# Performance work log

Measured on AMD Instinct MI355X. Metric: run time of the kernel, lower is better.

Reference implementation:

```python
import jax, jax.numpy as jnp
import numpy as np

B_, L_, DM = 2, 2048, 1024
DS, DC, EXP, HD = 128, 4, 2, 64
DI = EXP * DM              # 2048
NH = DI // HD              # 32 heads
CONV_DIM = DI + 2 * DS     # 2304
DIN = 2 * DI + 2 * DS + NH # 4384 (z, xBC, dt)
CS = 256                   # SSD chunk size
EPS = 1e-5


def setup_inputs() -> dict:
    key = jax.random.key(0)
    ks = jax.random.split(key, 8)
    s = 0.02
    x = jax.random.normal(ks[0], (B_, L_, DM), jnp.float32)
    norm_w = jnp.ones((DM,), jnp.float32)
    in_proj_w = jax.random.normal(ks[1], (DIN, DM), jnp.float32) * s
    conv_w = jax.random.normal(ks[2], (CONV_DIM, DC), jnp.float32) * 0.2
    conv_b = jnp.zeros((CONV_DIM,), jnp.float32)
    # inverse-softplus of dt ~ U(0.001, 0.1)
    dt_bias = jnp.log(jnp.expm1(jax.random.uniform(ks[3], (NH,), minval=0.001, maxval=0.1)))
    A_log = jnp.log(jax.random.uniform(ks[4], (NH,), minval=1.0, maxval=16.0))
    D = jnp.ones((NH,), jnp.float32)
    gnorm_w = jnp.ones((DI,), jnp.float32)
    out_proj_w = jax.random.normal(ks[5], (DM, DI), jnp.float32) * s
    return dict(x=x, norm_w=norm_w, in_proj_w=in_proj_w, conv_w=conv_w, conv_b=conv_b,
                dt_bias=dt_bias, A_log=A_log, D=D, gnorm_w=gnorm_w, out_proj_w=out_proj_w)


def _segsum(a):
    # a: [..., T] -> [..., T, T]; (i,j) = sum_{j<k<=i} a_k, -inf above diagonal
    T = a.shape[-1]
    cs = jnp.cumsum(a, -1)
    seg = cs[..., :, None] - cs[..., None, :]
    mask = jnp.tril(jnp.ones((T, T), bool))
    return jnp.where(mask, seg, -jnp.inf)


def _ssd(X, A, Bm, Cm):
    # X: [b,l,h,p] (= x*dt), A: [b,l,h] (= dt*a), Bm,Cm: [b,l,n] (ngroups=1)
    b, l, h, p = X.shape
    n, nc = Bm.shape[-1], l // CS
    X = X.reshape(b, nc, CS, h, p)
    A = A.reshape(b, nc, CS, h).transpose(0, 3, 1, 2)  # [b,h,c,s]
    Bm = Bm.reshape(b, nc, CS, n)
    Cm = Cm.reshape(b, nc, CS, n)
    Acs = jnp.cumsum(A, -1)                            # [b,h,c,s]
    Lmat = jnp.exp(_segsum(A))                         # [b,h,c,s,s]
    Y_diag = jnp.einsum('bcln,bcsn,bhcls,bcshp->bclhp', Cm, Bm, Lmat, X)
    decay_states = jnp.exp(Acs[..., -1:] - Acs)        # [b,h,c,s]
    states = jnp.einsum('bcln,bhcl,bclhp->bchpn', Bm, decay_states, X)
    states = jnp.concatenate([jnp.zeros_like(states[:, :1]), states], axis=1)  # [b,c+1,h,p,n]
    decay_chunk = jnp.exp(_segsum(jnp.pad(Acs[..., -1], ((0, 0), (0, 0), (1, 0)))))  # [b,h,c+1,c+1]
    states = jnp.einsum('bhzc,bchpn->bzhpn', decay_chunk, states)[:, :-1]
    Y_off = jnp.einsum('bcln,bchpn,bhcl->bclhp', Cm, states, jnp.exp(Acs))
    return (Y_diag + Y_off).reshape(b, l, h, p)


def _forward(x, norm_w, in_proj_w, conv_w, conv_b, dt_bias, A_log, D, gnorm_w, out_proj_w):
    b, l, _ = x.shape
    # outer RMSNorm
    xn = x * jax.lax.rsqrt(jnp.mean(x * x, -1, keepdims=True) + EPS) * norm_w
    zxbcdt = jnp.einsum('bld,ed->ble', xn, in_proj_w)
    z = zxbcdt[..., :DI]
    xBC = zxbcdt[..., DI:DI + CONV_DIM]
    dt = zxbcdt[..., -NH:]
    # causal depthwise conv1d + bias + silu
    pad = jnp.pad(xBC, ((0, 0), (DC - 1, 0), (0, 0)))
    conv = sum(pad[:, k:k + l, :] * conv_w[:, k] for k in range(DC)) + conv_b
    xBC = conv * jax.nn.sigmoid(conv)
    xs = xBC[..., :DI]
    Bm = xBC[..., DI:DI + DS]
    Cm = xBC[..., DI + DS:]
    dt = jax.nn.softplus(dt + dt_bias)                 # [b,l,h]
    A = -jnp.exp(A_log)                                # [h]
    xh = xs.reshape(b, l, NH, HD)
    y = _ssd(xh * dt[..., None], dt * A, Bm, Cm)
    y = y + D[None, None, :, None] * xh
    y = y.reshape(b, l, DI)
    # gated RMSNorm (norm_before_gate=False): rmsnorm(y * silu(z)) * w
    y = y * (z * jax.nn.sigmoid(z))
    y = y * jax.lax.rsqrt(jnp.mean(y * y, -1, keepdims=True) + EPS) * gnorm_w
    return x + jnp.einsum('bld,ed->ble', y, out_proj_w)


def reference(x, norm_w, in_proj_w, conv_w, conv_b, dt_bias, A_log, D, gnorm_w, out_proj_w):
    return _forward(x, norm_w, in_proj_w, conv_w, conv_b, dt_bias, A_log, D, gnorm_w, out_proj_w)
```

## Files before the change

### kernel.cpp

```cpp
#include <hip/hip_runtime.h>
#include <hip/hip_bf16.h>

#define BB      2
#define LSEQ    2048
#define DMODEL  1024
#define DSTATE  128
#define DCONV   4
#define HEADDIM 64
#define DINNER  2048
#define NHEADS  32
#define CONVD   2304
#define DINP    4384
#define CHUNK   256
#define NCH     8
#define NROWS   4096
#define EPSF    1e-5f
#define TPAD    264
#define WIPAD   4480

typedef __attribute__((ext_vector_type(8))) short bf16x8;
typedef __attribute__((ext_vector_type(4))) float f32x4;

#define ASYNC_COPY16(gptr, lptr) \
    __builtin_amdgcn_global_load_lds((const __attribute__((address_space(1))) void*)(gptr), \
                                     (__attribute__((address_space(3))) void*)(lptr), 16, 0, 0)

__device__ __forceinline__ ushort f2bf(float f) {
    __hip_bfloat16 h = __float2bfloat16(f);
    return *(ushort*)&h;
}
__device__ __forceinline__ float bf2f(ushort u) {
    return __uint_as_float(((unsigned)u) << 16);
}
__device__ __forceinline__ short fb(float f) { return (short)f2bf(f); }
__device__ __forceinline__ short tb(float f) { return (short)(__float_as_uint(f) >> 16); }

__global__ __launch_bounds__(256) void prologue_kernel(
    const float* __restrict__ x, const float* __restrict__ norm_w,
    const float* __restrict__ in_proj_w, const float* __restrict__ out_proj_w,
    const float* __restrict__ gnorm_w,
    ushort* __restrict__ xn_bf, ushort* __restrict__ wi_bf,
    ushort* __restrict__ wo_bf, float* __restrict__ ssq)
{
    int bid = blockIdx.x;
    if (bid < 4480) {
        long i4 = ((long)bid * 256 + threadIdx.x) * 4;
        int n = (int)(i4 >> 10);
        long k = i4 & 1023;
        ushort4 o;
        if (n < DINP) {
            float4 v = *(const float4*)(in_proj_w + ((long)n << 10) + k);
            o.x = f2bf(v.x); o.y = f2bf(v.y); o.z = f2bf(v.z); o.w = f2bf(v.w);
        } else { o.x = o.y = o.z = o.w = 0; }
        *(ushort4*)(wi_bf + i4) = o;
    } else if (bid < 6528) {
        long i4 = ((long)(bid - 4480) * 256 + threadIdx.x) * 4;
        int k = (int)(i4 & 2047);
        float4 v = *(const float4*)(out_proj_w + i4);
        float4 g = *(const float4*)(gnorm_w + k);
        ushort4 o;
        o.x = f2bf(v.x * g.x); o.y = f2bf(v.y * g.y);
        o.z = f2bf(v.z * g.z); o.w = f2bf(v.w * g.w);
        *(ushort4*)(wo_bf + i4) = o;
    } else if (bid < 10624) {
        int row = bid - 6528;
        const float* xr = x + (long)row * DMODEL;
        float4 v = *(const float4*)(xr + threadIdx.x * 4);
        float ss = v.x*v.x + v.y*v.y + v.z*v.z + v.w*v.w;
        for (int off = 32; off; off >>= 1) ss += __shfl_down(ss, off, 64);
        __shared__ float red[4];
        if ((threadIdx.x & 63) == 0) red[threadIdx.x >> 6] = ss;
        __syncthreads();
        float tot = red[0] + red[1] + red[2] + red[3];
        float scale = rsqrtf(tot / (float)DMODEL + EPSF);
        float4 wv = *(const float4*)(norm_w + threadIdx.x * 4);
        ushort4 o;
        o.x = f2bf(v.x * scale * wv.x); o.y = f2bf(v.y * scale * wv.y);
        o.z = f2bf(v.z * scale * wv.z); o.w = f2bf(v.w * scale * wv.w);
        *(ushort4*)(xn_bf + (long)row * DMODEL + threadIdx.x * 4) = o;
    } else {
        ssq[(bid - 10624) * 256 + threadIdx.x] = 0.f;
    }
}

__global__ __launch_bounds__(256, 3) void gemm_bf16_kernel(
    const ushort* __restrict__ A, int lda, long sA,
    const ushort* __restrict__ W, int ldw, long sW,
    void* __restrict__ Cout, int ldc, long sC, int c_bf16,
    const float* __restrict__ resid, const float* __restrict__ rowscale,
    int mtiles, int ntiles, int N, int K)
{
    __shared__ __align__(16) char smem[34816];
    ushort* As = (ushort*)smem;
    ushort* Bs = As + 128 * 64;
    ushort* tu = (ushort*)smem;
    float*  tf = (float*)smem;

    const int t = threadIdx.x;
    const int lane = t & 63;
    const int w = t >> 6;
    const int wm = w & 1, wn = w >> 1;
    const int lm = lane & 15, quad = lane >> 4;

    int pid = blockIdx.x;
    const int GM = 8;
    int width = GM * ntiles;
    int group = pid / width;
    int first_m = group * GM;
    int gsz = mtiles - first_m; if (gsz > GM) gsz = GM;
    int mt = first_m + (pid % width) % gsz;
    int nt = (pid % width) / gsz;
    const int m0 = mt * 128, n0 = nt * 128;

    A += (long)blockIdx.z * sA;
    W += (long)blockIdx.z * sW;

    const ushort* ga[4]; const ushort* gw[4];
#pragma unroll
    for (int i = 0; i < 4; ++i) {
        int s = i * 256 + t;
        int row = s >> 3;
        int kseg = (s & 7) ^ (row & 7);
        ga[i] = A + (long)(m0 + row) * lda + kseg * 8;
        gw[i] = W + (long)(n0 + row) * ldw + kseg * 8;
    }

    f32x4 acc[4][4];
    f32x4 zero4 = {0.f, 0.f, 0.f, 0.f};
#pragma unroll
    for (int i = 0; i < 4; ++i)
#pragma unroll
        for (int j = 0; j < 4; ++j) acc[i][j] = zero4;

    int arow8[4], arow7[4], brow8[4], brow7[4];
#pragma unroll
    for (int i = 0; i < 4; ++i) {
        int ar = wm * 64 + i * 16 + lm;
        arow8[i] = ar * 8; arow7[i] = ar & 7;
        int br = wn * 64 + i * 16 + lm;
        brow8[i] = br * 8; brow7[i] = br & 7;
    }

    for (int k0 = 0; k0 < K; k0 += 64) {
#pragma unroll
        for (int i = 0; i < 4; ++i) {
            ASYNC_COPY16(ga[i], &As[(i * 256 + w * 64) * 8]);
            ga[i] += 64;
        }
#pragma unroll
        for (int i = 0; i < 4; ++i) {
            ASYNC_COPY16(gw[i], &Bs[(i * 256 + w * 64) * 8]);
            gw[i] += 64;
        }
        __syncthreads();
#pragma unroll
        for (int ks = 0; ks < 2; ++ks) {
            bf16x8 af[4], bfr[4];
#pragma unroll
            for (int i = 0; i < 4; ++i)
                af[i]  = *(const bf16x8*)&As[(arow8[i] + ((ks * 4 + quad) ^ arow7[i])) * 8];
#pragma unroll
            for (int i = 0; i < 4; ++i)
                bfr[i] = *(const bf16x8*)&Bs[(brow8[i] + ((ks * 4 + quad) ^ brow7[i])) * 8];
#pragma unroll
            for (int im = 0; im < 4; ++im)
#pragma unroll
                for (int in = 0; in < 4; ++in)
                    acc[im][in] = __builtin_amdgcn_mfma_f32_16x16x32_bf16(
                        af[im], bfr[in], acc[im][in], 0, 0, 0);
        }
        __syncthreads();
    }

    if (c_bf16) {
        ushort* C = (ushort*)Cout + (long)blockIdx.z * sC;
#pragma unroll
        for (int mi = 0; mi < 4; ++mi)
#pragma unroll
            for (int ni = 0; ni < 4; ++ni) {
                int c = wn * 64 + ni * 16 + lm;
#pragma unroll
                for (int i = 0; i < 4; ++i) {
                    int r = wm * 64 + mi * 16 + quad * 4 + i;
                    tu[r * 136 + c] = f2bf(acc[mi][ni][i]);
                }
            }
        __syncthreads();
        int r = t >> 1, cb = (t & 1) * 64;
        long rowbase = (long)(m0 + r) * ldc + n0 + cb;
#pragma unroll
        for (int q = 0; q < 8; ++q) {
            int gcol = n0 + cb + q * 8;
            if (gcol < N)
                *(bf16x8*)(C + rowbase + q * 8) =
                    *(const bf16x8*)&tu[r * 136 + cb + q * 8];
        }
    } else {
        float* C = (float*)Cout + (long)blockIdx.z * sC;
#pragma unroll
        for (int p = 0; p < 2; ++p) {
            if (wm == p) {
#pragma unroll
                for (int mi = 0; mi < 4; ++mi)
#pragma unroll
                    for (int i = 0; i < 4; ++i) {
                        int r = mi * 16 + quad * 4 + i;
                        float s = 1.f;
                        if (rowscale)
                            s = rsqrtf(rowscale[m0 + p * 64 + r] * (1.f / (float)DINNER) + EPSF);
#pragma unroll
                        for (int ni = 0; ni < 4; ++ni) {
                            int c = wn * 64 + ni * 16 + lm;
                            tf[r * 132 + c] = acc[mi][ni][i] * s;
                        }
                    }
            }
            __syncthreads();
            int r2 = t >> 2, cb = (t & 3) * 32;
            long gbase = (long)(m0 + p * 64 + r2) * ldc + n0 + cb;
#pragma unroll
            for (int q = 0; q < 8; ++q) {
                float4 v = *(const float4*)&tf[r2 * 132 + cb + q * 4];
                if (resid) {
                    float4 rv = *(const float4*)(resid + gbase + q * 4);
                    v.x += rv.x; v.y += rv.y; v.z += rv.z; v.w += rv.w;
                }
                *(float4*)(C + gbase + q * 4) = v;
            }
            __syncthreads();
        }
    }
}

__global__ __launch_bounds__(256, 4) void gemm_bf16_s_kernel(
    const ushort* __restrict__ A, int lda, long sA,
    const ushort* __restrict__ W, int ldw, long sW,
    void* __restrict__ Cout, int ldc, long sC, int c_bf16,
    const float* __restrict__ resid, const float* __restrict__ rowscale,
    int mtiles, int ntiles, int N, int K)
{
    __shared__ __align__(16) char smem[24576];
    ushort* As = (ushort*)smem;
    ushort* Bs = As + 128 * 64;
    ushort* tu = (ushort*)smem;
    float*  tf = (float*)smem;

    const int t = threadIdx.x;
    const int lane = t & 63;
    const int w = t >> 6;
    const int wm = w & 1, wn = w >> 1;
    const int lm = lane & 15, quad = lane >> 4;

    int pid = blockIdx.x;
    const int GM = 8;
    int width = GM * ntiles;
    int group = pid / width;
    int first_m = group * GM;
    int gsz = mtiles - first_m; if (gsz > GM) gsz = GM;
    int mt = first_m + (pid % width) % gsz;
    int nt = (pid % width) / gsz;
    const int m0 = mt * 128, n0 = nt * 64;

    A += (long)blockIdx.z * sA;
    W += (long)blockIdx.z * sW;

    const ushort* ga[4]; const ushort* gw[2];
#pragma unroll
    for (int i = 0; i < 4; ++i) {
        int s = i * 256 + t;
        int row = s >> 3;
        int kseg = (s & 7) ^ (row & 7);
        ga[i] = A + (long)(m0 + row) * lda + kseg * 8;
    }
#pragma unroll
    for (int i = 0; i < 2; ++i) {
        int s = i * 256 + t;
        int row = s >> 3;
        int kseg = (s & 7) ^ (row & 7);
        gw[i] = W + (long)(n0 + row) * ldw + kseg * 8;
    }

    f32x4 acc[4][2];
    f32x4 zero4 = {0.f, 0.f, 0.f, 0.f};
#pragma unroll
    for (int i = 0; i < 4; ++i) { acc[i][0] = zero4; acc[i][1] = zero4; }

    int arow8[4], arow7[4], brow8[2], brow7[2];
#pragma unroll
    for (int i = 0; i < 4; ++i) {
        int ar = wm * 64 + i * 16 + lm;
        arow8[i] = ar * 8; arow7[i] = ar & 7;
    }
#pragma unroll
    for (int i = 0; i < 2; ++i) {
        int br = wn * 32 + i * 16 + lm;
        brow8[i] = br * 8; brow7[i] = br & 7;
    }

    for (int k0 = 0; k0 < K; k0 += 64) {
#pragma unroll
        for (int i = 0; i < 4; ++i) {
            ASYNC_COPY16(ga[i], &As[(i * 256 + w * 64) * 8]);
            ga[i] += 64;
        }
#pragma unroll
        for (int i = 0; i < 2; ++i) {
            ASYNC_COPY16(gw[i], &Bs[(i * 256 + w * 64) * 8]);
            gw[i] += 64;
        }
        __syncthreads();
#pragma unroll
        for (int ks = 0; ks < 2; ++ks) {
            bf16x8 af[4], bfr[2];
#pragma unroll
            for (int i = 0; i < 4; ++i)
                af[i]  = *(const bf16x8*)&As[(arow8[i] + ((ks * 4 + quad) ^ arow7[i])) * 8];
#pragma unroll
            for (int i = 0; i < 2; ++i)
                bfr[i] = *(const bf16x8*)&Bs[(brow8[i] + ((ks * 4 + quad) ^ brow7[i])) * 8];
#pragma unroll
            for (int im = 0; im < 4; ++im)
#pragma unroll
                for (int in = 0; in < 2; ++in)
                    acc[im][in] = __builtin_amdgcn_mfma_f32_16x16x32_bf16(
                        af[im], bfr[in], acc[im][in], 0, 0, 0);
        }
        __syncthreads();
    }

    if (c_bf16) {
        ushort* C = (ushort*)Cout + (long)blockIdx.z * sC;
#pragma unroll
        for (int mi = 0; mi < 4; ++mi)
#pragma unroll
            for (int ni = 0; ni < 2; ++ni) {
                int c = wn * 32 + ni * 16 + lm;
#pragma unroll
                for (int i = 0; i < 4; ++i) {
                    int r = wm * 64 + mi * 16 + quad * 4 + i;
                    tu[r * 72 + c] = f2bf(acc[mi][ni][i]);
                }
            }
        __syncthreads();
        int r = t >> 1, cb = (t & 1) * 32;
        long rowbase = (long)(m0 + r) * ldc + n0 + cb;
#pragma unroll
        for (int q = 0; q < 4; ++q) {
            int gcol = n0 + cb + q * 8;
            if (gcol < N)
                *(bf16x8*)(C + rowbase + q * 8) =
                    *(const bf16x8*)&tu[r * 72 + cb + q * 8];
        }
    } else {
        float* C = (float*)Cout + (long)blockIdx.z * sC;
#pragma unroll
        for (int p = 0; p < 2; ++p) {
            if (wm == p) {
#pragma unroll
                for (int mi = 0; mi < 4; ++mi)
#pragma unroll
                    for (int i = 0; i < 4; ++i) {
                        int r = mi * 16 + quad * 4 + i;
                        float s = 1.f;
                        if (rowscale)
                            s = rsqrtf(rowscale[m0 + p * 64 + r] * (1.f / (float)DINNER) + EPSF);
#pragma unroll
                        for (int ni = 0; ni < 2; ++ni) {
                            int c = wn * 32 + ni * 16 + lm;
                            tf[r * 68 + c] = acc[mi][ni][i] * s;
                        }
                    }
            }
            __syncthreads();
            int r2 = t >> 2, cb = (t & 3) * 16;
            long gbase = (long)(m0 + p * 64 + r2) * ldc + n0 + cb;
#pragma unroll
            for (int q = 0; q < 4; ++q) {
                float4 v = *(const float4*)&tf[r2 * 68 + cb + q * 4];
                if (resid) {
                    float4 rv = *(const float4*)(resid + gbase + q * 4);
                    v.x += rv.x; v.y += rv.y; v.z += rv.z; v.w += rv.w;
                }
                *(float4*)(C + gbase + q * 4) = v;
            }
            __syncthreads();
        }
    }
}

__device__ __forceinline__ void conv8_row(
    const ushort* __restrict__ zx, const float* __restrict__ cw,
    const float* __restrict__ cb, ushort* __restrict__ xBC_bf,
    int row, int l, int c)
{
    float4 cwv[8];
#pragma unroll
    for (int j = 0; j < 8; ++j) cwv[j] = *(const float4*)(cw + (c + j) * 4);
    float acc[8];
    {
        float4 b0 = *(const float4*)(cb + c);
        float4 b1 = *(const float4*)(cb + c + 4);
        acc[0] = b0.x; acc[1] = b0.y; acc[2] = b0.z; acc[3] = b0.w;
        acc[4] = b1.x; acc[5] = b1.y; acc[6] = b1.z; acc[7] = b1.w;
    }
#pragma unroll
    for (int k = 0; k < DCONV; ++k) {
        int ls = l + k - (DCONV - 1);
        if (ls >= 0) {
            const ushort* zr = zx + (long)(row + k - (DCONV - 1)) * DINP + DINNER + c;
            ushort4 a = *(const ushort4*)zr;
            ushort4 b = *(const ushort4*)(zr + 4);
            acc[0] += bf2f(a.x) * ((const float*)&cwv[0])[k];
            acc[1] += bf2f(a.y) * ((const float*)&cwv[1])[k];
            acc[2] += bf2f(a.z) * ((const float*)&cwv[2])[k];
            acc[3] += bf2f(a.w) * ((const float*)&cwv[3])[k];
            acc[4] += bf2f(b.x) * ((const float*)&cwv[4])[k];
            acc[5] += bf2f(b.y) * ((const float*)&cwv[5])[k];
            acc[6] += bf2f(b.z) * ((const float*)&cwv[6])[k];
            acc[7] += bf2f(b.w) * ((const float*)&cwv[7])[k];
        }
    }
    ushort o[8];
#pragma unroll
    for (int j = 0; j < 8; ++j)
        o[j] = f2bf(acc[j] / (1.f + __expf(-acc[j])));
    ushort* dst = xBC_bf + (long)row * CONVD + c;
    *(ushort4*)dst = *(ushort4*)&o[0];
    *(ushort4*)(dst + 4) = *(ushort4*)&o[4];
}

__global__ __launch_bounds__(256) void conv_acs_kernel(
    const ushort* __restrict__ zx, const float* __restrict__ cw,
    const float* __restrict__ cb, ushort* __restrict__ xBC_bf,
    const float* __restrict__ dt_bias, const float* __restrict__ A_log,
    float* __restrict__ dtv, float* __restrict__ Acs)
{
    int bid = blockIdx.x;
    int t = threadIdx.x;
    if (bid < NROWS) {
        int row = bid;
        int l = row & (LSEQ - 1);
        conv8_row(zx, cw, cb, xBC_bf, row, l, t * 8);
        if (t < 32)
            conv8_row(zx, cw, cb, xBC_bf, row, l, 2048 + t * 8);
    } else {
        __shared__ float buf[2 * CHUNK];
        int idx = bid - NROWS;
        int bc = idx >> 5, h = idx & 31;
        int l = t;
        int row = bc * CHUNK + l;
        float v = bf2f(zx[(long)row * DINP + (DINP - NHEADS) + h]) + dt_bias[h];
        float d = (v > 20.f) ? v : log1pf(__expf(v));
        dtv[row * NHEADS + h] = d;
        float a = -d * __expf(A_log[h]);
        buf[l] = a; __syncthreads();
        int src = 0;
        for (int off = 1; off < CHUNK; off <<= 1) {
            float vv = buf[src * CHUNK + l];
            if (l >= off) vv += buf[src * CHUNK + l - off];
            buf[(src ^ 1) * CHUNK + l] = vv;
            __syncthreads();
            src ^= 1;
        }
        Acs[(bc * NHEADS + h) * CHUNK + l] = buf[src * CHUNK + l];
    }
}

__global__ __launch_bounds__(256) void prep_b_kernel(
    const ushort* __restrict__ xBC_bf, ushort* __restrict__ Bt)
{
    int bc = blockIdx.x, half = blockIdx.y;
    int t = threadIdx.x;
    int row0 = bc * CHUNK;
    __shared__ ushort tB[64 * TPAD];
    int src_c0 = DINNER + half * 64;
    for (int iter = 0; iter < 8; ++iter) {
        int l = iter * 32 + (t >> 3);
        int cc = (t & 7) * 8;
        ushort u[8];
        *(ushort4*)&u[0] = *(const ushort4*)(xBC_bf + (long)(row0 + l) * CONVD + src_c0 + cc);
        *(ushort4*)&u[4] = *(const ushort4*)(xBC_bf + (long)(row0 + l) * CONVD + src_c0 + cc + 4);
#pragma unroll
        for (int j = 0; j < 8; ++j) tB[(cc + j) * TPAD + l] = u[j];
    }
    __syncthreads();
    int r = t >> 2, seg = (t & 3) * 64;
    ushort* dst = Bt + ((long)bc * DSTATE + half * 64 + r) * CHUNK + seg;
    const ushort* s1 = &tB[r * TPAD + seg];
#pragma unroll
    for (int q = 0; q < 16; ++q)
        *(ushort4*)(dst + q * 4) = *(const ushort4*)(s1 + q * 4);
}

__global__ __launch_bounds__(256) void chunk_state_mfma_kernel(
    const ushort* __restrict__ xBC_bf, const ushort* __restrict__ Bt,
    const float* __restrict__ dtv, const float* __restrict__ acs,
    ushort* __restrict__ state)
{
    int bc = blockIdx.x, h = blockIdx.y;
    int t = threadIdx.x, lane = t & 63, w = t >> 6;
    int lm = lane & 15, quad = lane >> 4;
    int row0 = bc * CHUNK;
    __shared__ ushort xt[64 * TPAD];
    __shared__ float cl[CHUNK];
    {
        float a = acs[(bc * NHEADS + h) * CHUNK + t];
        float T = acs[(bc * NHEADS + h) * CHUNK + CHUNK - 1];
        cl[t] = __expf(T - a) * dtv[(row0 + t) * NHEADS + h];
    }
    __syncthreads();
    for (int iter = 0; iter < 8; ++iter) {
        int l = iter * 32 + (t >> 3);
        int cc = (t & 7) * 8;
        ushort u[8];
        *(ushort4*)&u[0] = *(const ushort4*)(xBC_bf + (long)(row0 + l) * CONVD + h * HEADDIM + cc);
        *(ushort4*)&u[4] = *(const ushort4*)(xBC_bf + (long)(row0 + l) * CONVD + h * HEADDIM + cc + 4);
        float sc = cl[l];
#pragma unroll
        for (int j = 0; j < 8; ++j)
            xt[(cc + j) * TPAD + l] = (ushort)tb(bf2f(u[j]) * sc);
    }
    __syncthreads();

    const ushort* Bb = Bt + (long)bc * DSTATE * CHUNK;
    f32x4 acc[4][2];
    f32x4 zero4 = {0.f, 0.f, 0.f, 0.f};
#pragma unroll
    for (int i = 0; i < 4; ++i) { acc[i][0] = zero4; acc[i][1] = zero4; }

    for (int kt = 0; kt < 8; ++kt) {
        int k = kt * 32 + quad * 8;
        bf16x8 af[4], bfr[2];
#pragma unroll
        for (int mi = 0; mi < 4; ++mi)
            af[mi] = *(const bf16x8*)&xt[(mi * 16 + lm) * TPAD + k];
#pragma unroll
        for (int nj = 0; nj < 2; ++nj)
            bfr[nj] = *(const bf16x8*)(Bb + (long)(w * 32 + nj * 16 + lm) * CHUNK + k);
#pragma unroll
        for (int mi = 0; mi < 4; ++mi)
#pragma unroll
            for (int nj = 0; nj < 2; ++nj)
                acc[mi][nj] = __builtin_amdgcn_mfma_f32_16x16x32_bf16(
                    af[mi], bfr[nj], acc[mi][nj], 0, 0, 0);
    }
    ushort* sp = state + (long)(bc * NHEADS + h) * (DSTATE * HEADDIM);
#pragma unroll
    for (int mi = 0; mi < 4; ++mi)
#pragma unroll
        for (int nj = 0; nj < 2; ++nj) {
            int n = w * 32 + nj * 16 + lm;
#pragma unroll
            for (int i = 0; i < 4; ++i) {
                int p = mi * 16 + quad * 4 + i;
                sp[p * DSTATE + n] = f2bf(acc[mi][nj][i]);
            }
        }
}

__global__ __launch_bounds__(256) void state_scan_kernel(
    ushort* __restrict__ state, const float* __restrict__ Acs)
{
    long flat = (long)blockIdx.x * 256 + threadIdx.x;
    int e = (int)(flat & 8191);
    int bh = (int)(flat >> 13);
    int b = bh >> 5, h = bh & 31;
    float S = 0.f;
    for (int c = 0; c < NCH; ++c) {
        int bc = b * NCH + c;
        long idx = ((long)(bc * NHEADS + h)) * 8192 + e;
        float T = Acs[(bc * NHEADS + h) * CHUNK + CHUNK - 1];
        float tmp = bf2f(state[idx]);
        state[idx] = f2bf(S);
        S = S * __expf(T) + tmp;
    }
}

__global__ __launch_bounds__(256) void ssd_y_mfma_kernel(
    const ushort* __restrict__ xBC_bf, const ushort* __restrict__ G2b,
    const float* __restrict__ acs, const ushort* __restrict__ state,
    const ushort* __restrict__ zxb, const float* __restrict__ dtv,
    const float* __restrict__ Dh, ushort* __restrict__ ybf,
    float* __restrict__ ssq)
{
    int bc = blockIdx.x, h = blockIdx.y;
    int t = threadIdx.x, lane = t & 63, w = t >> 6;
    int lm = lane & 15, quad = lane >> 4;
    int row0 = bc * CHUNK;
    __shared__ ushort xt[64 * TPAD];
    __shared__ float acs_s[CHUNK];
    __shared__ float dl[CHUNK];
    acs_s[t] = acs[(bc * NHEADS + h) * CHUNK + t];
    dl[t] = dtv[(row0 + t) * NHEADS + h];
    __syncthreads();
    for (int iter = 0; iter < 8; ++iter) {
        int l = iter * 32 + (t >> 3);
        int cc = (t & 7) * 8;
        ushort u[8];
        *(ushort4*)&u[0] = *(const ushort4*)(xBC_bf + (long)(row0 + l) * CONVD + h * HEADDIM + cc);
        *(ushort4*)&u[4] = *(const ushort4*)(xBC_bf + (long)(row0 + l) * CONVD + h * HEADDIM + cc + 4);
        float sd = dl[l];
#pragma unroll
        for (int j = 0; j < 8; ++j)
            xt[(cc + j) * TPAD + l] = (ushort)tb(bf2f(u[j]) * sd);
    }
    __syncthreads();

    int lbase = w * 64;
    float acs_l[4], eAl[4];
#pragma unroll
    for (int mi = 0; mi < 4; ++mi) {
        acs_l[mi] = acs_s[lbase + mi * 16 + lm];
        eAl[mi] = __expf(acs_l[mi]);
    }
    f32x4 acc[4][4];
    f32x4 zero4 = {0.f, 0.f, 0.f, 0.f};
#pragma unroll
    for (int i = 0; i < 4; ++i)
#pragma unroll
        for (int j = 0; j < 4; ++j) acc[i][j] = zero4;

    const ushort* g2 = G2b + (long)bc * (CHUNK * CHUNK);

    for (int ks = 0; ks <= 2 * w + 1; ++ks) {
        int sq = ks * 32 + quad * 8;
        bf16x8 bfr[4];
#pragma unroll
        for (int ni = 0; ni < 4; ++ni)
            bfr[ni] = *(const bf16x8*)&xt[(ni * 16 + lm) * TPAD + sq];
        float base = acs_s[sq];
        float e8[8];
        e8[0] = 1.f;
#pragma unroll
        for (int j = 1; j < 8; ++j)
            e8[j] = __expf(fminf(base - acs_s[sq + j], 80.f));
#pragma unroll
        for (int mi = 0; mi < 4; ++mi) {
            int lmin = lbase + mi * 16;
            if (ks * 32 > lmin + 15) continue;
            int lv = lmin + lm;
            float em = __expf(fminf(acs_l[mi] - base, 0.f));
            bf16x8 g8 = *(const bf16x8*)(g2 + (long)lv * CHUNK + sq);
            bf16x8 af;
#pragma unroll
            for (int j = 0; j < 8; ++j) {
                float v = bf2f((ushort)g8[j]) * (em * e8[j]);
                af[j] = (sq + j > lv) ? (short)0 : tb(v);
            }
#pragma unroll
            for (int ni = 0; ni < 4; ++ni)
                acc[mi][ni] = __builtin_amdgcn_mfma_f32_16x16x32_bf16(
                    af, bfr[ni], acc[mi][ni], 0, 0, 0);
        }
    }

    const ushort* sp = state + (long)(bc * NHEADS + h) * (DSTATE * HEADDIM);
    const ushort* Cb = xBC_bf + (long)row0 * CONVD + DINNER + DSTATE;
    for (int kt = 0; kt < 4; ++kt) {
        int n0 = kt * 32 + quad * 8;
        bf16x8 bfr[4];
#pragma unroll
        for (int ni = 0; ni < 4; ++ni)
            bfr[ni] = *(const bf16x8*)(sp + (long)(ni * 16 + lm) * DSTATE + n0);
#pragma unroll
        for (int mi = 0; mi < 4; ++mi) {
            int lv = lbase + mi * 16 + lm;
            bf16x8 cu = *(const bf16x8*)(Cb + (long)lv * CONVD + n0);
            bf16x8 ce;
            float e = eAl[mi];
#pragma unroll
            for (int j = 0; j < 8; ++j) ce[j] = tb(bf2f((ushort)cu[j]) * e);
#pragma unroll
            for (int ni = 0; ni < 4; ++ni)
                acc[mi][ni] = __builtin_amdgcn_mfma_f32_16x16x32_bf16(
                    ce, bfr[ni], acc[mi][ni], 0, 0, 0);
        }
    }

    float Dv = Dh[h];
#pragma unroll
    for (int mi = 0; mi < 4; ++mi)
#pragma unroll
        for (int i = 0; i < 4; ++i) {
            int l = lbase + mi * 16 + quad * 4 + i;
            long row = row0 + l;
            float ps = 0.f;
#pragma unroll
            for (int ni = 0; ni < 4; ++ni) {
                int p = ni * 16 + lm;
                float xh = bf2f(xBC_bf[row * CONVD + h * HEADDIM + p]);
                float z = bf2f(zxb[row * DINP + h * HEADDIM + p]);
                float o = (acc[mi][ni][i] + Dv * xh) * (z / (1.f + __expf(-z)));
                ps += o * o;
                ybf[row * DINNER + h * HEADDIM + p] = f2bf(o);
            }
#pragma unroll
            for (int m = 1; m < 16; m <<= 1) ps += __shfl_xor(ps, m, 64);
            if (lm == 0) atomicAdd(&ssq[row], ps);
        }
}

extern "C" void kernel_launch(void* const* d_in, const int* in_sizes, int n_in,
                              void* d_out, int out_size, void* d_ws, size_t ws_size,
                              hipStream_t stream)
{
    (void)in_sizes; (void)n_in; (void)out_size; (void)ws_size;
    const float* x          = (const float*)d_in[0];
    const float* norm_w     = (const float*)d_in[1];
    const float* in_proj_w  = (const float*)d_in[2];
    const float* conv_w     = (const float*)d_in[3];
    const float* conv_b     = (const float*)d_in[4];
    const float* dt_bias    = (const float*)d_in[5];
    const float* A_log      = (const float*)d_in[6];
    const float* Dh         = (const float*)d_in[7];
    const float* gnorm_w    = (const float*)d_in[8];
    const float* out_proj_w = (const float*)d_in[9];
    float* out = (float*)d_out;
    float* ws = (float*)d_ws;

    float* zxb_f   = ws;
    float* xbc_f   = zxb_f   + 8978432;
    float* dtv     = xbc_f   + 4718592;
    float* acs     = dtv     + 131072;
    float* g2_f    = acs     + 131072;
    float* state_f = g2_f    + 524288;
    float* bt_f    = state_f + 2097152;
    float* regU    = bt_f    + 262144;
    float* wo_f    = regU    + 4390912;
    float* ssq     = wo_f    + 1048576;

    ushort* zxb_bf = (ushort*)zxb_f;
    ushort* xBC_bf = (ushort*)xbc_f;
    ushort* G2b    = (ushort*)g2_f;
    ushort* state  = (ushort*)state_f;
    ushort* Bt     = (ushort*)bt_f;
    ushort* xn_bf  = (ushort*)regU;
    ushort* wi_bf  = (ushort*)(regU + 2097152);
    ushort* ybf    = (ushort*)regU;
    ushort* wo_bf  = (ushort*)wo_f;

    prologue_kernel<<<dim3(10640), 256, 0, stream>>>(
        x, norm_w, in_proj_w, out_proj_w, gnorm_w, xn_bf, wi_bf, wo_bf, ssq);

    gemm_bf16_kernel<<<dim3(32 * 35), 256, 0, stream>>>(
        xn_bf, DMODEL, 0, wi_bf, DMODEL, 0,
        zxb_bf, DINP, 0, 1, nullptr, nullptr, 32, 35, DINP, DMODEL);

    conv_acs_kernel<<<dim3(NROWS + BB * NCH * NHEADS), 256, 0, stream>>>(
        zxb_bf, conv_w, conv_b, xBC_bf, dt_bias, A_log, dtv, acs);

    prep_b_kernel<<<dim3(BB * NCH, 2), 256, 0, stream>>>(xBC_bf, Bt);

    gemm_bf16_s_kernel<<<dim3(8, 1, BB * NCH), 256, 0, stream>>>(
        xBC_bf + DINNER + DSTATE, CONVD, (long)CHUNK * CONVD,
        xBC_bf + DINNER, CONVD, (long)CHUNK * CONVD,
        G2b, CHUNK, (long)CHUNK * CHUNK, 1, nullptr, nullptr, 2, 4, CHUNK, DSTATE);

    chunk_state_mfma_kernel<<<dim3(BB * NCH, NHEADS), 256, 0, stream>>>(
        xBC_bf, Bt, dtv, acs, state);

    state_scan_kernel<<<dim3(BB * NHEADS * 8192 / 256), 256, 0, stream>>>(state, acs);

    ssd_y_mfma_kernel<<<dim3(BB * NCH, NHEADS), 256, 0, stream>>>(
        xBC_bf, G2b, acs, state, zxb_bf, dtv, Dh, ybf, ssq);

    gemm_bf16_s_kernel<<<dim3(32 * 16), 256, 0, stream>>>(
        ybf, DINNER, 0, wo_bf, DINNER, 0,
        out, DMODEL, 0, 0, x, ssq, 32, 16, DMODEL, DINNER);
}
```

Before: 298.1 us.

## Split-K out_proj GEMM with atomic accumulation and XCD-aware block swizzle

The output projection GEMM is split four ways along K (512 each) using blockIdx.z, and each split adds its rowscaled partial into the output with float atomicAdd. The prologue now seeds the output with x as the residual. This is meant to raise the block count for a GEMM that had only 512 tiles. Separately, both GEMM kernels remap block IDs so consecutive tiles land on the same XCD for better L2 reuse. Atomics add memory traffic, make the summation order nondeterministic, and skip the LDS-staged coalesced store.

```diff
diff --git a/kernel.cpp b/kernel.cpp
--- a/kernel.cpp
+++ b/kernel.cpp
@@ -16,7 +16,6 @@
 #define NROWS   4096
 #define EPSF    1e-5f
 #define TPAD    264
-#define WIPAD   4480
 
 typedef __attribute__((ext_vector_type(8))) short bf16x8;
 typedef __attribute__((ext_vector_type(4))) float f32x4;
@@ -32,15 +31,19 @@
 __device__ __forceinline__ float bf2f(ushort u) {
     return __uint_as_float(((unsigned)u) << 16);
 }
-__device__ __forceinline__ short fb(float f) { return (short)f2bf(f); }
 __device__ __forceinline__ short tb(float f) { return (short)(__float_as_uint(f) >> 16); }
+
+__device__ __forceinline__ int xcd_swizzle(int pid, int nwg) {
+    return ((nwg & 7) == 0) ? (pid & 7) * (nwg >> 3) + (pid >> 3) : pid;
+}
 
 __global__ __launch_bounds__(256) void prologue_kernel(
     const float* __restrict__ x, const float* __restrict__ norm_w,
     const float* __restrict__ in_proj_w, const float* __restrict__ out_proj_w,
     const float* __restrict__ gnorm_w,
     ushort* __restrict__ xn_bf, ushort* __restrict__ wi_bf,
-    ushort* __restrict__ wo_bf, float* __restrict__ ssq)
+    ushort* __restrict__ wo_bf, float* __restrict__ ssq,
+    float* __restrict__ out)
 {
     int bid = blockIdx.x;
     if (bid < 4480) {
@@ -78,8 +81,11 @@
         o.x = f2bf(v.x * scale * wv.x); o.y = f2bf(v.y * scale * wv.y);
         o.z = f2bf(v.z * scale * wv.z); o.w = f2bf(v.w * scale * wv.w);
         *(ushort4*)(xn_bf + (long)row * DMODEL + threadIdx.x * 4) = o;
+    } else if (bid < 10640) {
+        ssq[(bid - 10624) * 256 + threadIdx.x] = 0.f;
     } else {
-        ssq[(bid - 10624) * 256 + threadIdx.x] = 0.f;
+        long i4 = ((long)(bid - 10640) * 256 + threadIdx.x) * 4;
+        *(float4*)(out + i4) = *(const float4*)(x + i4);
     }
 }
 
@@ -102,7 +108,7 @@
     const int wm = w & 1, wn = w >> 1;
     const int lm = lane & 15, quad = lane >> 4;
 
-    int pid = blockIdx.x;
+    int pid = xcd_swizzle(blockIdx.x, gridDim.x);
     const int GM = 8;
     int width = GM * ntiles;
     int group = pid / width;
@@ -251,7 +257,7 @@
     const int wm = w & 1, wn = w >> 1;
     const int lm = lane & 15, quad = lane >> 4;
 
-    int pid = blockIdx.x;
+    int pid = xcd_swizzle(blockIdx.x, gridDim.x);
     const int GM = 8;
     int width = GM * ntiles;
     int group = pid / width;
@@ -328,7 +334,7 @@
         __syncthreads();
     }
 
-    if (c_bf16) {
+    if (c_bf16 == 1) {
         ushort* C = (ushort*)Cout + (long)blockIdx.z * sC;
 #pragma unroll
         for (int mi = 0; mi < 4; ++mi)
@@ -351,6 +357,20 @@
                 *(bf16x8*)(C + rowbase + q * 8) =
                     *(const bf16x8*)&tu[r * 72 + cb + q * 8];
         }
+    } else if (c_bf16 == 2) {
+        float* C = (float*)Cout;
+#pragma unroll
+        for (int mi = 0; mi < 4; ++mi)
+#pragma unroll
+            for (int i = 0; i < 4; ++i) {
+                int r = m0 + wm * 64 + mi * 16 + quad * 4 + i;
+                float s = rsqrtf(rowscale[r] * (1.f / (float)DINNER) + EPSF);
+#pragma unroll
+                for (int ni = 0; ni < 2; ++ni) {
+                    int c = n0 + wn * 32 + ni * 16 + lm;
+                    atomicAdd(&C[(long)r * ldc + c], acc[mi][ni][i] * s);
+                }
+            }
     } else {
         float* C = (float*)Cout + (long)blockIdx.z * sC;
 #pragma unroll
@@ -739,8 +759,8 @@
     ushort* ybf    = (ushort*)regU;
     ushort* wo_bf  = (ushort*)wo_f;
 
-    prologue_kernel<<<dim3(10640), 256, 0, stream>>>(
-        x, norm_w, in_proj_w, out_proj_w, gnorm_w, xn_bf, wi_bf, wo_bf, ssq);
+    prologue_kernel<<<dim3(14736), 256, 0, stream>>>(
+        x, norm_w, in_proj_w, out_proj_w, gnorm_w, xn_bf, wi_bf, wo_bf, ssq, out);
 
     gemm_bf16_kernel<<<dim3(32 * 35), 256, 0, stream>>>(
         xn_bf, DMODEL, 0, wi_bf, DMODEL, 0,
@@ -764,7 +784,7 @@
     ssd_y_mfma_kernel<<<dim3(BB * NCH, NHEADS), 256, 0, stream>>>(
         xBC_bf, G2b, acs, state, zxb_bf, dtv, Dh, ybf, ssq);
 
-    gemm_bf16_s_kernel<<<dim3(32 * 16), 256, 0, stream>>>(
-        ybf, DINNER, 0, wo_bf, DINNER, 0,
-        out, DMODEL, 0, 0, x, ssq, 32, 16, DMODEL, DINNER);
-}
+    gemm_bf16_s_kernel<<<dim3(32 * 16, 1, 4), 256, 0, stream>>>(
+        ybf, DINNER, 512, wo_bf, DINNER, 512,
+        out, DMODEL, 0, 2, nullptr, ssq, 32, 16, DMODEL, 512);
+}
```

Result: slower. 317.2 us (+6.4%).
